# Optimization experiments

Measured on AMD Instinct MI355X. Metric: run time of the kernel, lower is better.

The kernel has to match this reference:

```python
import jax, jax.numpy as jnp
import numpy as np

GROUP_SIZE = 128  # quantization group size along K


def setup_inputs() -> dict:
    key = jax.random.key(0)
    k1, k2, k3, k4 = jax.random.split(key, 4)
    B, S, K = 2, 2048, 4096
    N = 11008
    num_groups = K // GROUP_SIZE
    x = jax.random.normal(k1, (B, S, K), dtype=jnp.float32)
    # int8 quantized weights, stored as int32 for portability (values in [-128, 127])
    qw = jax.random.randint(k2, (N, K), -128, 128, dtype=jnp.int32)
    # per-group scales (positive, small, like amax/127)
    sw = jax.random.uniform(k3, (N, num_groups), dtype=jnp.float32, minval=1e-4, maxval=0.02)
    bias = jax.random.normal(k4, (N,), dtype=jnp.float32)
    return {"x": x, "qw": qw, "sw": sw, "bias": bias}


def reference(x, qw, sw, bias):
    # x: [..., K], qw: [N, K] int8-valued, sw: [N, K//GROUP_SIZE], bias: [N]
    N, K = qw.shape
    num_groups = K // GROUP_SIZE
    # per-group dequantize: w[n, g, j] = qw[n, g, j] * sw[n, g]
    w_dequant = (qw.reshape(N, num_groups, GROUP_SIZE).astype(jnp.float32)
                 * sw[:, :, None]).reshape(N, K)
    x_dtype = x.dtype
    y = jnp.einsum('...k,nk->...n', x.astype(jnp.float32), w_dequant).astype(x_dtype)
    y = y + bias
    return y
```

## Files before the change

kernel.cpp:

```cpp
#include <hip/hip_runtime.h>


typedef __attribute__((ext_vector_type(8))) short short8;
typedef __attribute__((ext_vector_type(4))) float floatx4;

__device__ __forceinline__ unsigned short f2bf_rne(float f) {
  union { float f; unsigned int u; } c;
  c.f = f;
  unsigned int u = c.u;
  u += 0x7FFFu + ((u >> 16) & 1u);
  return (unsigned short)(u >> 16);
}

__global__ void prep_x_kernel(const float* __restrict__ x,
                              short* __restrict__ xb, long nchunks) {
  long stride = (long)gridDim.x * blockDim.x;
  for (long c = (long)blockIdx.x * blockDim.x + threadIdx.x;
       c < nchunks; c += stride) {
    const float4* p = (const float4*)(x + c * 8);
    float4 a = p[0], b = p[1];
    short8 o;
    o[0] = (short)f2bf_rne(a.x); o[1] = (short)f2bf_rne(a.y);
    o[2] = (short)f2bf_rne(a.z); o[3] = (short)f2bf_rne(a.w);
    o[4] = (short)f2bf_rne(b.x); o[5] = (short)f2bf_rne(b.y);
    o[6] = (short)f2bf_rne(b.z); o[7] = (short)f2bf_rne(b.w);
    *(short8*)(xb + c * 8) = o;
  }
}

__global__ void prep_w_kernel(const int* __restrict__ qw,
                              const float* __restrict__ sw,
                              short* __restrict__ wb, long nchunks,
                              int kc, int kcshift, int gc, int gcshift,
                              int ngroups) {
  long stride = (long)gridDim.x * blockDim.x;
  for (long c = (long)blockIdx.x * blockDim.x + threadIdx.x;
       c < nchunks; c += stride) {
    int n, kch;
    if (kcshift >= 0) {
      n = (int)(c >> kcshift);
      kch = (int)(c & (long)(kc - 1));
    } else {
      n = (int)(c / kc);
      kch = (int)(c - (long)n * kc);
    }
    int g = (gcshift >= 0) ? (kch >> gcshift) : (kch / gc);
    float s = sw[(long)n * ngroups + g];
    const int* q = qw + c * 8;
    int4 q0 = *(const int4*)q;
    int4 q1 = *(const int4*)(q + 4);
    short8 o;
    o[0] = (short)f2bf_rne((float)q0.x * s);
    o[1] = (short)f2bf_rne((float)q0.y * s);
    o[2] = (short)f2bf_rne((float)q0.z * s);
    o[3] = (short)f2bf_rne((float)q0.w * s);
    o[4] = (short)f2bf_rne((float)q1.x * s);
    o[5] = (short)f2bf_rne((float)q1.y * s);
    o[6] = (short)f2bf_rne((float)q1.z * s);
    o[7] = (short)f2bf_rne((float)q1.w * s);
    *(short8*)(wb + c * 8) = o;
  }
}

#define BM 128
#define BN 128
#define BK 32


__device__ __forceinline__ void stage_tile(const short* __restrict__ Ag,
                                           const short* __restrict__ Bg,
                                           int k0, int K,
                                           short* Adst, short* Bdst,
                                           int t, int srow, int scol) {
#pragma unroll
  for (int i = 0; i < 2; ++i)
    __builtin_amdgcn_global_load_lds(
        (const __attribute__((address_space(1))) void*)(
            Ag + (long)(i * 64 + srow) * K + k0 + scol),
        (__attribute__((address_space(3))) void*)(Adst + i * 64 * BK + t * 8),
        16, 0, 0);
#pragma unroll
  for (int i = 0; i < 2; ++i)
    __builtin_amdgcn_global_load_lds(
        (const __attribute__((address_space(1))) void*)(
            Bg + (long)(i * 64 + srow) * K + k0 + scol),
        (__attribute__((address_space(3))) void*)(Bdst + i * 64 * BK + t * 8),
        16, 0, 0);
}

__global__ __launch_bounds__(256, 4) void gemm_bt_kernel(
    const short* __restrict__ Xb,
    const short* __restrict__ Wb,
    const float* __restrict__ bias,
    float* __restrict__ Y,
    int M, int N, int K) {
  __shared__ short As[2][BM * BK];
  __shared__ short Bs[2][BN * BK];

  const int t = threadIdx.x;
  const int wave = t >> 6;
  const int lane = t & 63;
  const int wm = wave >> 1;
  const int wn = wave & 1;
  const int quad = lane >> 4;
  const int l16 = lane & 15;

  const int gn = gridDim.x, gm = gridDim.y;
  int mt, nt;
  if ((gm & 7) == 0) {
    int stripe = gm >> 3;
    int bid = blockIdx.y * gn + blockIdx.x;
    int xcd = bid & 7;
    int q = bid >> 3;
    int msub = q % stripe;
    nt = q / stripe;
    mt = xcd * stripe + msub;
  } else {
    mt = blockIdx.y; nt = blockIdx.x;
  }
  const int tileM = mt * BM;
  const int tileN = nt * BN;

  floatx4 acc[4][4];
#pragma unroll
  for (int i = 0; i < 4; i++)
#pragma unroll
    for (int j = 0; j < 4; j++) acc[i][j] = {0.f, 0.f, 0.f, 0.f};

  const int srow = t >> 2;
  const int scol = ((t & 3) ^ ((t >> 3) & 3)) * 8;

  const short* Ag = Xb + (long)tileM * K;
  const short* Bg = Wb + (long)tileN * K;

  const int cswz = (quad ^ ((l16 >> 1) & 3)) * 8;

  stage_tile(Ag, Bg, 0, K, &As[0][0], &Bs[0][0], t, srow, scol);
  __syncthreads();

  int cur = 0;
  for (int k0 = 0; k0 < K; k0 += BK, cur ^= 1) {
    if (k0 + BK < K)
      stage_tile(Ag, Bg, k0 + BK, K, &As[cur ^ 1][0], &Bs[cur ^ 1][0],
                 t, srow, scol);

    const short* Aw = &As[cur][0] + wm * 64 * BK;
    const short* Bw = &Bs[cur][0] + wn * 64 * BK;
    short8 af[4], bf[4];
#pragma unroll
    for (int i = 0; i < 4; i++)
      af[i] = *(const short8*)(Aw + (i * 16 + l16) * BK + cswz);
#pragma unroll
    for (int j = 0; j < 4; j++)
      bf[j] = *(const short8*)(Bw + (j * 16 + l16) * BK + cswz);

#pragma unroll
    for (int i = 0; i < 4; i++)
#pragma unroll
      for (int j = 0; j < 4; j++)
        acc[i][j] = __builtin_amdgcn_mfma_f32_16x16x32_bf16(af[i], bf[j],
                                                            acc[i][j], 0, 0, 0);
    __syncthreads();
  }

  const int mbase = tileM + wm * 64;
  const int nbase = tileN + wn * 64;
#pragma unroll
  for (int i = 0; i < 4; i++) {
#pragma unroll
    for (int j = 0; j < 4; j++) {
      int n = nbase + j * 16 + l16;
      float bv = bias[n];
#pragma unroll
      for (int r = 0; r < 4; r++) {
        int m = mbase + i * 16 + quad * 4 + r;
        Y[(long)m * N + n] = acc[i][j][r] + bv;
      }
    }
  }
}

__global__ void naive_kernel(const float* __restrict__ x,
                             const int* __restrict__ qw,
                             const float* __restrict__ sw,
                             const float* __restrict__ bias,
                             float* __restrict__ y,
                             int M, int N, int K, int G) {
  long idx = (long)blockIdx.x * blockDim.x + threadIdx.x;
  if (idx >= (long)M * N) return;
  int m = (int)(idx / N), n = (int)(idx % N);
  int ng = K / G;
  float acc = 0.f;
  for (int g = 0; g < ng; g++) {
    float s = sw[(long)n * ng + g];
    float part = 0.f;
    for (int k = g * G; k < (g + 1) * G; k++)
      part += x[(long)m * K + k] * (float)qw[(long)n * K + k];
    acc += part * s;
  }
  y[idx] = acc + bias[n];
}

extern "C" void kernel_launch(void* const* d_in, const int* in_sizes, int n_in,
                              void* d_out, int out_size, void* d_ws, size_t ws_size,
                              hipStream_t stream) {
  const float* x = (const float*)d_in[0];
  const int* qw = (const int*)d_in[1];
  const float* sw = (const float*)d_in[2];
  const float* bias = (const float*)d_in[3];
  float* y = (float*)d_out;

  const int N = in_sizes[3];
  const int K = in_sizes[1] / N;
  const int M = in_sizes[0] / K;
  const int ngroups = in_sizes[2] / N;
  const int G = K / ngroups;

  const long MK = (long)M * K;
  const long NK = (long)N * K;
  const size_t need = (size_t)(MK + NK) * sizeof(short);

  if (ws_size < need || (M % BM) || (N % BN) || (K % BK) || (G % 8)) {
    long total = (long)M * N;
    naive_kernel<<<(unsigned)((total + 255) / 256), 256, 0, stream>>>(
        x, qw, sw, bias, y, M, N, K, G);
    return;
  }

  short* xb = (short*)d_ws;
  short* wb = xb + MK;

  const int kc = K / 8;
  const int gc = G / 8;
  int kcshift = ((kc & (kc - 1)) == 0) ? __builtin_ctz((unsigned)kc) : -1;
  int gcshift = ((gc & (gc - 1)) == 0) ? __builtin_ctz((unsigned)gc) : -1;

  prep_x_kernel<<<2048, 256, 0, stream>>>(x, xb, MK / 8);
  prep_w_kernel<<<2048, 256, 0, stream>>>(qw, sw, wb, NK / 8,
                                          kc, kcshift, gc, gcshift, ngroups);

  dim3 grid((unsigned)(N / BN), (unsigned)(M / BM));
  gemm_bt_kernel<<<grid, 256, 0, stream>>>(xb, wb, bias, y, M, N, K);
}
```

Before: 741.2 us.

## Switch GEMM to single-buffered BK=64 tiles with 8-way XOR swizzle

Replaces the double-buffered BK=32 LDS pipeline with a single buffer of BK=64. Each iteration loads the full tile, synchronizes, then runs two K-substeps of MFMAs. The LDS layout uses an 8-chunk XOR swizzle to avoid bank conflicts. This halves the number of loop iterations and barriers per K, but gives up the overlap of the next tile's global loads with compute.

```diff
diff --git a/kernel.cpp b/kernel.cpp
--- a/kernel.cpp
+++ b/kernel.cpp
@@ -64,29 +64,7 @@
 
 #define BM 128
 #define BN 128
-#define BK 32
-
-
-__device__ __forceinline__ void stage_tile(const short* __restrict__ Ag,
-                                           const short* __restrict__ Bg,
-                                           int k0, int K,
-                                           short* Adst, short* Bdst,
-                                           int t, int srow, int scol) {
-#pragma unroll
-  for (int i = 0; i < 2; ++i)
-    __builtin_amdgcn_global_load_lds(
-        (const __attribute__((address_space(1))) void*)(
-            Ag + (long)(i * 64 + srow) * K + k0 + scol),
-        (__attribute__((address_space(3))) void*)(Adst + i * 64 * BK + t * 8),
-        16, 0, 0);
-#pragma unroll
-  for (int i = 0; i < 2; ++i)
-    __builtin_amdgcn_global_load_lds(
-        (const __attribute__((address_space(1))) void*)(
-            Bg + (long)(i * 64 + srow) * K + k0 + scol),
-        (__attribute__((address_space(3))) void*)(Bdst + i * 64 * BK + t * 8),
-        16, 0, 0);
-}
+#define BK 64
 
 __global__ __launch_bounds__(256, 4) void gemm_bt_kernel(
     const short* __restrict__ Xb,
@@ -94,8 +72,8 @@
     const float* __restrict__ bias,
     float* __restrict__ Y,
     int M, int N, int K) {
-  __shared__ short As[2][BM * BK];
-  __shared__ short Bs[2][BN * BK];
+  __shared__ short As[BM * BK];
+  __shared__ short Bs[BN * BK];
 
   const int t = threadIdx.x;
   const int wave = t >> 6;
@@ -127,39 +105,55 @@
 #pragma unroll
     for (int j = 0; j < 4; j++) acc[i][j] = {0.f, 0.f, 0.f, 0.f};
 
-  const int srow = t >> 2;
-  const int scol = ((t & 3) ^ ((t >> 3) & 3)) * 8;
-
   const short* Ag = Xb + (long)tileM * K;
   const short* Bg = Wb + (long)tileN * K;
 
-  const int cswz = (quad ^ ((l16 >> 1) & 3)) * 8;
-
-  stage_tile(Ag, Bg, 0, K, &As[0][0], &Bs[0][0], t, srow, scol);
-  __syncthreads();
-
-  int cur = 0;
-  for (int k0 = 0; k0 < K; k0 += BK, cur ^= 1) {
-    if (k0 + BK < K)
-      stage_tile(Ag, Bg, k0 + BK, K, &As[cur ^ 1][0], &Bs[cur ^ 1][0],
-                 t, srow, scol);
-
-    const short* Aw = &As[cur][0] + wm * 64 * BK;
-    const short* Bw = &Bs[cur][0] + wn * 64 * BK;
-    short8 af[4], bf[4];
-#pragma unroll
-    for (int i = 0; i < 4; i++)
-      af[i] = *(const short8*)(Aw + (i * 16 + l16) * BK + cswz);
-#pragma unroll
-    for (int j = 0; j < 4; j++)
-      bf[j] = *(const short8*)(Bw + (j * 16 + l16) * BK + cswz);
-
-#pragma unroll
-    for (int i = 0; i < 4; i++)
+  const int c0 = (quad ^ (l16 & 7)) << 3;
+
+  for (int k0 = 0; k0 < K; k0 += BK) {
+#pragma unroll
+    for (int jj = 0; jj < 4; ++jj) {
+      const int c = (jj << 8) | t;
+      const int r = c >> 3;
+      const int g = (c & 7) ^ (r & 7);
+      __builtin_amdgcn_global_load_lds(
+          (const __attribute__((address_space(1))) void*)(
+              Ag + (long)r * K + k0 + (g << 3)),
+          (__attribute__((address_space(3))) void*)(As + (c << 3)),
+          16, 0, 0);
+    }
+#pragma unroll
+    for (int jj = 0; jj < 4; ++jj) {
+      const int c = (jj << 8) | t;
+      const int r = c >> 3;
+      const int g = (c & 7) ^ (r & 7);
+      __builtin_amdgcn_global_load_lds(
+          (const __attribute__((address_space(1))) void*)(
+              Bg + (long)r * K + k0 + (g << 3)),
+          (__attribute__((address_space(3))) void*)(Bs + (c << 3)),
+          16, 0, 0);
+    }
+    __syncthreads();
+
+    const short* Aw = As + wm * 64 * BK;
+    const short* Bw = Bs + wn * 64 * BK;
+#pragma unroll
+    for (int s = 0; s < 2; ++s) {
+      const int cs = c0 ^ (s << 5);
+      short8 af[4], bf[4];
+#pragma unroll
+      for (int i = 0; i < 4; i++)
+        af[i] = *(const short8*)(Aw + (i * 16 + l16) * BK + cs);
 #pragma unroll
       for (int j = 0; j < 4; j++)
-        acc[i][j] = __builtin_amdgcn_mfma_f32_16x16x32_bf16(af[i], bf[j],
-                                                            acc[i][j], 0, 0, 0);
+        bf[j] = *(const short8*)(Bw + (j * 16 + l16) * BK + cs);
+#pragma unroll
+      for (int i = 0; i < 4; i++)
+#pragma unroll
+        for (int j = 0; j < 4; j++)
+          acc[i][j] = __builtin_amdgcn_mfma_f32_16x16x32_bf16(
+              af[i], bf[j], acc[i][j], 0, 0, 0);
+    }
     __syncthreads();
   }
 
```

Result: faster. 670.3 us (-9.6%).
